# Optimization experiments

Measured on AMD Instinct MI355X. Metric: run time of the kernel, lower is better.

Reference implementation:

```python
import jax, jax.numpy as jnp
import numpy as np

B, D = 8192, 128
REGULARIZE = 0.01


def setup_inputs() -> dict:
    key = jax.random.key(0)
    ks = jax.random.split(key, 8)
    s = 1.0 / np.sqrt(D)
    X = jax.random.normal(ks[0], (B, D), dtype=jnp.float32)
    y = jax.random.randint(ks[1], (B,), 0, 100, dtype=jnp.int64 if jax.config.read('jax_enable_x64') else jnp.int32)
    W1 = jax.random.normal(ks[2], (D, D), dtype=jnp.float32) * s
    b1 = jnp.zeros((D,), dtype=jnp.float32)
    W2 = jax.random.normal(ks[3], (D, D), dtype=jnp.float32) * s
    b2 = jnp.zeros((D,), dtype=jnp.float32)
    W3 = jax.random.normal(ks[4], (D, D), dtype=jnp.float32) * s
    b3 = jnp.zeros((D,), dtype=jnp.float32)
    return {"X": X, "W1": W1, "b1": b1, "W2": W2, "b2": b2, "W3": W3, "b3": b3, "y": y}


def _mapper(X, W1, b1, W2, b2, W3, b3):
    h = jax.nn.relu(X @ W1 + b1)
    h = jax.nn.relu(h @ W2 + b2)
    return h @ W3 + b3  # no activation on last layer


def reference(X, W1, b1, W2, b2, W3, b3, y):
    h = _mapper(X, W1, b1, W2, b2, W3, b3)          # (B, D)
    avg_dist = jnp.mean(h ** 2)
    # squared euclidean all-pairs via GEMM trick: ||a-b||^2 = |a|^2 + |b|^2 - 2 a.b
    sq = jnp.sum(h ** 2, axis=-1)                   # (B,)
    dist = jnp.maximum(sq[:, None] + sq[None, :] - 2.0 * (h @ h.T), 0.0)  # (B, B)
    neq = (y[None, :] != y[:, None]).astype(h.dtype)
    eq = 1.0 - neq
    # -mean(neq * log(1.01 - exp(-d))) - mean(eq * log(exp(-d))) ; log(exp(-d)) = -d
    loss = -jnp.mean(neq * jnp.log(1.01 - jnp.exp(-dist))) + jnp.mean(eq * dist)
    loss = loss + REGULARIZE * avg_dist
    return loss
```

## Files before the change

### kernel.cpp

```cpp
#include <hip/hip_runtime.h>
#include <stdint.h>

#define D 128
#define B_ROWS 8192
#define NT 64
#define NPAIRBLK (NT * (NT + 1) / 2)
#define LW 136

typedef __bf16 bf16x8 __attribute__((ext_vector_type(8)));
typedef float f32x4 __attribute__((ext_vector_type(4)));

__global__ __launch_bounds__(256, 2) void mlp_kernel(
    const float* __restrict__ X,
    const float* __restrict__ W1, const float* __restrict__ b1,
    const float* __restrict__ W2, const float* __restrict__ b2,
    const float* __restrict__ W3, const float* __restrict__ b3,
    unsigned short* __restrict__ hb, float* __restrict__ sq)
{
    __shared__ unsigned short actA[16 * LW];
    __shared__ unsigned short actB[16 * LW];

    const int t = threadIdx.x;
    const int lane = t & 63;
    const int w = t >> 6;
    const int row0 = blockIdx.x * 16;
    const int ll = lane & 15;
    const int q  = lane >> 4;
    const int nb0 = w * 32;

    {
        const int r  = t >> 4;
        const int c8 = (t & 15) * 8;
        const float* xp = X + (size_t)(row0 + r) * D + c8;
        float4 v0 = *(const float4*)(xp);
        float4 v1 = *(const float4*)(xp + 4);
        bf16x8 u;
        u[0] = (__bf16)v0.x; u[1] = (__bf16)v0.y; u[2] = (__bf16)v0.z; u[3] = (__bf16)v0.w;
        u[4] = (__bf16)v1.x; u[5] = (__bf16)v1.y; u[6] = (__bf16)v1.z; u[7] = (__bf16)v1.w;
        *(bf16x8*)(actA + r * LW + c8) = u;
    }
    __syncthreads();

    auto layer = [&](const unsigned short* __restrict__ actIn,
                     unsigned short* __restrict__ actOut,
                     const float* __restrict__ Wg,
                     const float* __restrict__ bg, bool do_relu) {
        f32x4 acc0 = {0.f, 0.f, 0.f, 0.f};
        f32x4 acc1 = {0.f, 0.f, 0.f, 0.f};
        #pragma unroll
        for (int kk = 0; kk < 4; ++kk) {
            bf16x8 a = *(const bf16x8*)(actIn + ll * LW + kk * 32 + q * 8);
            float wv0[8], wv1[8];
            #pragma unroll
            for (int j = 0; j < 8; ++j) {
                const int kg = kk * 32 + q * 8 + j;
                wv0[j] = Wg[kg * D + nb0 + ll];
                wv1[j] = Wg[kg * D + nb0 + 16 + ll];
            }
            bf16x8 b0, b1;
            #pragma unroll
            for (int j = 0; j < 8; ++j) {
                b0[j] = (__bf16)wv0[j];
                b1[j] = (__bf16)wv1[j];
            }
            acc0 = __builtin_amdgcn_mfma_f32_16x16x32_bf16(a, b0, acc0, 0, 0, 0);
            acc1 = __builtin_amdgcn_mfma_f32_16x16x32_bf16(a, b1, acc1, 0, 0, 0);
        }
        const float bb0 = bg[nb0 + ll];
        const float bb1 = bg[nb0 + 16 + ll];
        #pragma unroll
        for (int rr = 0; rr < 4; ++rr) {
            const int m = q * 4 + rr;
            float v0 = acc0[rr] + bb0;
            float v1 = acc1[rr] + bb1;
            if (do_relu) { v0 = fmaxf(v0, 0.f); v1 = fmaxf(v1, 0.f); }
            *(__bf16*)(actOut + m * LW + nb0 + ll)      = (__bf16)v0;
            *(__bf16*)(actOut + m * LW + nb0 + 16 + ll) = (__bf16)v1;
        }
    };

    layer(actA, actB, W1, b1, true);
    __syncthreads();
    layer(actB, actA, W2, b2, true);
    __syncthreads();
    layer(actA, actB, W3, b3, false);
    __syncthreads();

    {
        const int r  = t >> 4;
        const int c8 = (t & 15) * 8;
        bf16x8 hv = *(const bf16x8*)(actB + r * LW + c8);
        *(bf16x8*)(hb + (size_t)(row0 + r) * D + c8) = hv;
        float ps = 0.f;
        #pragma unroll
        for (int j = 0; j < 8; ++j) {
            float f = (float)hv[j];
            ps = fmaf(f, f, ps);
        }
        #pragma unroll
        for (int m = 1; m < 16; m <<= 1) ps += __shfl_xor(ps, m, 64);
        if ((t & 15) == 0) sq[row0 + r] = ps;
    }
}

__global__ __launch_bounds__(256, 2) void pair_kernel(
    const unsigned short* __restrict__ hb, const float* __restrict__ sq,
    const int* __restrict__ y, float* __restrict__ partials)
{
    __shared__ unsigned short ldsA[128 * 128];
    __shared__ unsigned short ldsB[128 * 128];
    __shared__ float sA[128], sB[128];
    __shared__ int yA[128], yB[128];
    __shared__ float red[4];

    const int t = threadIdx.x;
    const int lane = t & 63;
    const int w = t >> 6;

    int b = blockIdx.x, ti = 0;
    while (b >= NT - ti) { b -= NT - ti; ++ti; }
    const int tj = ti + b;
    const int i0 = ti * 128, j0 = tj * 128;

    if (t < 128) { sA[t] = sq[i0 + t]; yA[t] = y[i0 + t]; }
    else { int u = t - 128; sB[u] = sq[j0 + u]; yB[u] = y[j0 + u]; }

    #pragma unroll
    for (int it = 0; it < 16; ++it) {
        const int fbase = w * 1024 + it * 64;
        const int f = fbase + lane;
        const int tile = fbase >> 11;
        const int r = (f >> 4) & 127;
        const int c = f & 15;
        const int gc = c ^ (r & 15);
        const unsigned short* src =
            hb + (size_t)((tile ? j0 : i0) + r) * D + gc * 8;
        unsigned short* dstbase =
            (tile ? ldsB : ldsA) + (size_t)(fbase & 2047) * 8;
        __builtin_amdgcn_global_load_lds(
            (const __attribute__((address_space(1))) void*)src,
            (__attribute__((address_space(3))) void*)dstbase, 16, 0, 0);
    }
    __syncthreads();

    f32x4 acc[4][4];
    const f32x4 z4 = {0.f, 0.f, 0.f, 0.f};
    #pragma unroll
    for (int a = 0; a < 4; ++a)
        #pragma unroll
        for (int c = 0; c < 4; ++c) acc[a][c] = z4;

    const int wr = w >> 1, wc = w & 1;
    const int lh = lane >> 4;
    const int ll = lane & 15;

    #pragma unroll
    for (int kk = 0; kk < 4; ++kk) {
        bf16x8 af[4], bfr[4];
        const int clog = kk * 4 + lh;
        const int phys = clog ^ ll;
        #pragma unroll
        for (int tr = 0; tr < 4; ++tr) {
            const int rowl = wr * 64 + tr * 16 + ll;
            af[tr] = *(const bf16x8*)(ldsA + rowl * 128 + phys * 8);
        }
        #pragma unroll
        for (int tc = 0; tc < 4; ++tc) {
            const int rowl = wc * 64 + tc * 16 + ll;
            bfr[tc] = *(const bf16x8*)(ldsB + rowl * 128 + phys * 8);
        }
        #pragma unroll
        for (int tr = 0; tr < 4; ++tr)
            #pragma unroll
            for (int tc = 0; tc < 4; ++tc)
                acc[tr][tc] = __builtin_amdgcn_mfma_f32_16x16x32_bf16(
                    af[tr], bfr[tc], acc[tr][tc], 0, 0, 0);
    }

    float si[16]; int yi[16];
    #pragma unroll
    for (int tr = 0; tr < 4; ++tr)
        #pragma unroll
        for (int rr = 0; rr < 4; ++rr) {
            const int iloc = wr * 64 + tr * 16 + lh * 4 + rr;
            si[tr * 4 + rr] = sA[iloc];
            yi[tr * 4 + rr] = yA[iloc];
        }
    float sj[4]; int yj[4];
    #pragma unroll
    for (int tc = 0; tc < 4; ++tc) {
        const int jloc = wc * 64 + tc * 16 + ll;
        sj[tc] = sB[jloc]; yj[tc] = yB[jloc];
    }

    float s = 0.f;
    #pragma unroll
    for (int tr = 0; tr < 4; ++tr)
        #pragma unroll
        for (int rr = 0; rr < 4; ++rr) {
            const float sii = si[tr * 4 + rr];
            const int   yii = yi[tr * 4 + rr];
            #pragma unroll
            for (int tc = 0; tc < 4; ++tc) {
                const float dot = acc[tr][tc][rr];
                float d = fmaxf(fmaf(-2.f, dot, sii + sj[tc]), 0.f);
                float e = __builtin_amdgcn_exp2f(d * -1.442695041f);
                float nlg = fmaf(e, fmaf(e, 0.49014802f, 0.99009901f), -0.00995033f);
                s += (yii != yj[tc]) ? nlg : d;
            }
        }

    #pragma unroll
    for (int m = 1; m < 64; m <<= 1) s += __shfl_xor(s, m, 64);
    if (lane == 0) red[w] = s;
    __syncthreads();
    if (t == 0) {
        const float wgt = (ti == tj) ? 1.f : 2.f;
        partials[blockIdx.x] = wgt * (red[0] + red[1] + red[2] + red[3]);
    }
}

__global__ __launch_bounds__(256) void reduce_kernel(
    const float* __restrict__ partials, const float* __restrict__ sq,
    float* __restrict__ out)
{
    __shared__ float r1[4], r3[4];
    const int t = threadIdx.x;
    const int lane = t & 63;
    const int w = t >> 6;
    float a1 = 0.f, a3 = 0.f;
    for (int i = t; i < NPAIRBLK; i += 256) a1 += partials[i];
    for (int i = t; i < B_ROWS; i += 256) a3 += sq[i];
    #pragma unroll
    for (int m = 1; m < 64; m <<= 1) {
        a1 += __shfl_xor(a1, m, 64);
        a3 += __shfl_xor(a3, m, 64);
    }
    if (lane == 0) { r1[w] = a1; r3[w] = a3; }
    __syncthreads();
    if (t == 0) {
        const float A1 = r1[0] + r1[1] + r1[2] + r1[3];
        const float A3 = r3[0] + r3[1] + r3[2] + r3[3];
        const float invB2 = 1.0f / (8192.0f * 8192.0f);
        out[0] = A1 * invB2 + 0.01f * A3 / (8192.0f * 128.0f);
    }
}

extern "C" void kernel_launch(void* const* d_in, const int* in_sizes, int n_in,
                              void* d_out, int out_size, void* d_ws, size_t ws_size,
                              hipStream_t stream) {
    (void)in_sizes; (void)n_in; (void)out_size; (void)ws_size;
    const float* X  = (const float*)d_in[0];
    const float* W1 = (const float*)d_in[1];
    const float* b1 = (const float*)d_in[2];
    const float* W2 = (const float*)d_in[3];
    const float* b2 = (const float*)d_in[4];
    const float* W3 = (const float*)d_in[5];
    const float* b3 = (const float*)d_in[6];
    const int*   y  = (const int*)d_in[7];

    char* ws = (char*)d_ws;
    unsigned short* hb = (unsigned short*)ws;
    float* sq = (float*)(ws + (size_t)B_ROWS * D * 2);
    float* partials = (float*)(ws + (size_t)B_ROWS * D * 2 + (size_t)B_ROWS * 4);

    mlp_kernel<<<B_ROWS / 16, 256, 0, stream>>>(X, W1, b1, W2, b2, W3, b3, hb, sq);
    pair_kernel<<<NPAIRBLK, 256, 0, stream>>>(hb, sq, y, partials);
    reduce_kernel<<<1, 256, 0, stream>>>(partials, sq, (float*)d_out);
}
```

Measured before the change: 110.9 us.

## Load pair-kernel MFMA fragments directly from global memory instead of LDS

Removes the 64KB LDS staging of the two 128x128 bf16 tiles in the pair kernel and has each wave read its A/B MFMA fragments straight from global memory (L2/L1). This frees LDS so occupancy can rise, and the launch bound is raised to 4 blocks per CU. The cost is redundant global reads, since each row fragment is fetched by two waves, and less coalesced 16-byte loads that now depend on cache hits.

```diff
diff --git a/kernel.cpp b/kernel.cpp
--- a/kernel.cpp
+++ b/kernel.cpp
@@ -103,12 +103,10 @@
     }
 }
 
-__global__ __launch_bounds__(256, 2) void pair_kernel(
+__global__ __launch_bounds__(256, 4) void pair_kernel(
     const unsigned short* __restrict__ hb, const float* __restrict__ sq,
     const int* __restrict__ y, float* __restrict__ partials)
 {
-    __shared__ unsigned short ldsA[128 * 128];
-    __shared__ unsigned short ldsB[128 * 128];
     __shared__ float sA[128], sB[128];
     __shared__ int yA[128], yB[128];
     __shared__ float red[4];
@@ -124,23 +122,6 @@
 
     if (t < 128) { sA[t] = sq[i0 + t]; yA[t] = y[i0 + t]; }
     else { int u = t - 128; sB[u] = sq[j0 + u]; yB[u] = y[j0 + u]; }
-
-    #pragma unroll
-    for (int it = 0; it < 16; ++it) {
-        const int fbase = w * 1024 + it * 64;
-        const int f = fbase + lane;
-        const int tile = fbase >> 11;
-        const int r = (f >> 4) & 127;
-        const int c = f & 15;
-        const int gc = c ^ (r & 15);
-        const unsigned short* src =
-            hb + (size_t)((tile ? j0 : i0) + r) * D + gc * 8;
-        unsigned short* dstbase =
-            (tile ? ldsB : ldsA) + (size_t)(fbase & 2047) * 8;
-        __builtin_amdgcn_global_load_lds(
-            (const __attribute__((address_space(1))) void*)src,
-            (__attribute__((address_space(3))) void*)dstbase, 16, 0, 0);
-    }
     __syncthreads();
 
     f32x4 acc[4][4];
@@ -154,21 +135,18 @@
     const int lh = lane >> 4;
     const int ll = lane & 15;
 
+    const unsigned short* Arow = hb + (size_t)(i0 + wr * 64 + ll) * D + lh * 8;
+    const unsigned short* Brow = hb + (size_t)(j0 + wc * 64 + ll) * D + lh * 8;
+
     #pragma unroll
     for (int kk = 0; kk < 4; ++kk) {
         bf16x8 af[4], bfr[4];
-        const int clog = kk * 4 + lh;
-        const int phys = clog ^ ll;
-        #pragma unroll
-        for (int tr = 0; tr < 4; ++tr) {
-            const int rowl = wr * 64 + tr * 16 + ll;
-            af[tr] = *(const bf16x8*)(ldsA + rowl * 128 + phys * 8);
-        }
-        #pragma unroll
-        for (int tc = 0; tc < 4; ++tc) {
-            const int rowl = wc * 64 + tc * 16 + ll;
-            bfr[tc] = *(const bf16x8*)(ldsB + rowl * 128 + phys * 8);
-        }
+        #pragma unroll
+        for (int tr = 0; tr < 4; ++tr)
+            af[tr] = *(const bf16x8*)(Arow + (size_t)tr * 16 * D + kk * 32);
+        #pragma unroll
+        for (int tc = 0; tc < 4; ++tc)
+            bfr[tc] = *(const bf16x8*)(Brow + (size_t)tc * 16 * D + kk * 32);
         #pragma unroll
         for (int tr = 0; tr < 4; ++tr)
             #pragma unroll
```

Measured after the change: 124.4 us. +12.1%, slower.
